# Kernel tuning notes

Hardware: AMD Instinct MI355X
Metric: run time of the kernel (lower is better)

Reference implementation:

```python
import jax, jax.numpy as jnp
import numpy as np

N, E, F, EF, D, G = 25000, 100000, 32, 8, 64, 1000


def setup_inputs() -> dict:
    key = jax.random.key(0)
    ks = jax.random.split(key, 32)
    p = lambda k, shape: (jax.random.normal(k, shape, jnp.float32) * 0.05)
    inp = {
        "x": jax.random.normal(ks[0], (N, F), jnp.float32),
        "edge_index": jax.random.randint(ks[1], (2, E), 0, N, jnp.int64 if jax.config.jax_enable_x64 else jnp.int32),
        "edge_attr": jax.random.uniform(ks[2], (E, EF), jnp.float32),
        "batch": jnp.sort(jax.random.randint(ks[3], (N,), 0, G, jnp.int32)),
        # lin0
        "W0": p(ks[4], (F, D)), "b0": p(ks[5], (D,)),
        # edge MLP: Linear(EF, D) -> ReLU -> Linear(D, D*D)
        "We1": p(ks[6], (EF, D)), "be1": p(ks[7], (D,)),
        "We2": p(ks[8], (D, D * D)), "be2": p(ks[9], (D * D,)),
        # NNConv root weight + bias
        "Wroot": p(ks[10], (D, D)), "bconv": p(ks[11], (D,)),
        # GRU (single layer): gate order r, z, n
        "Wi": p(ks[12], (3 * D, D)), "Wh": p(ks[13], (3 * D, D)),
        "bi": p(ks[14], (3 * D,)), "bh": p(ks[15], (3 * D,)),
        # heads
        "W11": p(ks[16], (D, D)), "b11": p(ks[17], (D,)),
        "W12": p(ks[18], (D, D)), "b12": p(ks[19], (D,)),
        "W13": p(ks[20], (D, 1)), "b13": p(ks[21], (1,)),
        "W21": p(ks[22], (D, D)), "b21": p(ks[23], (D,)),
        "W22": p(ks[24], (D, D)), "b22": p(ks[25], (D,)),
        "W23": p(ks[26], (D, 1)), "b23": p(ks[27], (1,)),
    }
    return inp


def reference(x, edge_index, edge_attr, batch,
              W0, b0, We1, be1, We2, be2, Wroot, bconv,
              Wi, Wh, bi, bh,
              W11, b11, W12, b12, W13, b13,
              W21, b21, W22, b22, W23, b23):
    src, dst = edge_index[0], edge_index[1]
    # lin0 + relu
    x1 = jax.nn.relu(x @ W0 + b0)                      # [N, D]
    h = x1                                              # GRU hidden init
    # NNConv: dynamic per-edge weight via edge MLP
    ew = (jax.nn.relu(edge_attr @ We1 + be1) @ We2 + be2).reshape(E, D, D)
    msg = jnp.einsum('ei,eio->eo', x1[src], ew)        # per-edge matmul
    agg = jax.ops.segment_sum(msg, dst, num_segments=N)
    x2 = jax.nn.relu(x1 @ Wroot + agg + bconv)         # [N, D]
    # GRU single step (torch gate order: r, z, n)
    gi = x2 @ Wi.T + bi
    gh = h @ Wh.T + bh
    r = jax.nn.sigmoid(gi[:, :D] + gh[:, :D])
    z = jax.nn.sigmoid(gi[:, D:2 * D] + gh[:, D:2 * D])
    n = jnp.tanh(gi[:, 2 * D:] + r * gh[:, 2 * D:])
    hn = (1.0 - z) * n + z * h                          # [N, D]
    # graph pooling (scatter_add over batch)
    pooled = jax.ops.segment_sum(hn, batch, num_segments=G)  # [G, D]
    # two MLP heads
    x_1 = jax.nn.relu(pooled @ W11 + b11)
    x_1 = jax.nn.relu(x_1 @ W12 + b12)
    x_1 = x_1 @ W13 + b13
    x_2 = jax.nn.relu(pooled @ W21 + b21)
    x_2 = jax.nn.relu(x_2 @ W22 + b22)
    x_2 = x_2 @ W23 + b23
    return jnp.concatenate([x_1, x_2], axis=1)          # [G, 2]
```

## Files before the change

### kernel.cpp

```cpp
#include <hip/hip_runtime.h>
#include <hip/hip_bf16.h>

#define NN 25000
#define NE 100000
#define FIN 32
#define DD 64
#define NG 1000

typedef unsigned short u16;
typedef __attribute__((ext_vector_type(8))) short short8;
typedef __attribute__((ext_vector_type(4))) float f32x4;

__device__ __forceinline__ float b2f(u16 u) {
    union { unsigned int i; float f; } v; v.i = ((unsigned int)u) << 16; return v.f;
}
__device__ __forceinline__ u16 f2b(float f) {
    __hip_bfloat16 h = __float2bfloat16(f);
    return __builtin_bit_cast(u16, h);
}
__device__ __forceinline__ bool idx_is_i64(const int* e) {
    return (e[1] == 0) & (e[3] == 0) & (e[5] == 0) & (e[7] == 0) & (e[9] == 0);
}
__device__ __forceinline__ int ld_src(const int* e, int i, bool i64) {
    return i64 ? e[2 * i] : e[i];
}
__device__ __forceinline__ int ld_dst(const int* e, int i, bool i64) {
    return i64 ? e[2 * (NE + i)] : e[NE + i];
}

__global__ __launch_bounds__(256) void k_pre(const float* __restrict__ x,
                                             const float* __restrict__ W0,
                                             const float* __restrict__ b0,
                                             u16* __restrict__ x1b,
                                             const float* __restrict__ We2,
                                             const float* __restrict__ be2,
                                             float* __restrict__ agg,
                                             float* __restrict__ pooled,
                                             u16* __restrict__ Bt2) {
    __shared__ float sW[FIN * DD];
    __shared__ float sx[4 * FIN];
    if (blockIdx.x < 6250) {
        int tid = threadIdx.x;
        for (int i = tid; i < FIN * DD; i += 256) sW[i] = W0[i];
        int nbase = blockIdx.x * 4;
        for (int i = tid; i < 4 * FIN; i += 256) {
            int nl = i >> 5, f = i & 31;
            int n = nbase + nl;
            sx[i] = (n < NN) ? x[n * FIN + f] : 0.f;
        }
        __syncthreads();
        int lane = tid & 63, nl = tid >> 6;
        int n = nbase + nl;
        if (n < NN) {
            float acc = b0[lane];
            #pragma unroll
            for (int f = 0; f < FIN; f++) acc += sx[nl * FIN + f] * sW[f * DD + lane];
            x1b[n * DD + lane] = f2b(fmaxf(acc, 0.f));
        }
    } else {
        int tid = (blockIdx.x - 6250) * 256 + threadIdx.x;
        int stride = 1024 * 256;
        for (int idx = tid; idx < 65 * 4096; idx += stride) {
            int kc = idx >> 12;
            int rem = idx & 4095;
            int f = rem >> 9;
            int ln = (rem >> 3) & 63;
            int j = idx & 7;
            int s = f >> 2, c = f & 3;
            int o = c * 16 + (ln & 15);
            int r = kc * 64 + s * 32 + (ln >> 4) * 8 + j;
            float v = (r < 4096) ? We2[(r >> 6) * 4096 + (r & 63) * 64 + o]
                                 : be2[(r - 4096) * 64 + o];
            Bt2[idx] = f2b(v);
        }
        for (int idx = tid; idx < NN * DD; idx += stride) agg[idx] = 0.f;
        for (int idx = tid; idx < NG * DD; idx += stride) pooled[idx] = 0.f;
    }
}

__global__ __launch_bounds__(512, 4) void k_msg(const float* __restrict__ ea,
                                                const int* __restrict__ eidx,
                                                const float* __restrict__ We1,
                                                const float* __restrict__ be1,
                                                const u16* __restrict__ x1b,
                                                const u16* __restrict__ Bt2,
                                                float* __restrict__ agg) {
    __shared__ __align__(16) u16 sX[128 * 72];
    __shared__ __align__(16) float sT[64 * 128];
    __shared__ float sWe1[8 * 64];
    __shared__ float sbe1[64];
    __shared__ int sDst[128];
    const int tid = threadIdx.x;
    const int lane = tid & 63, wv = tid >> 6;
    const int ll = lane & 15, quad = lane >> 4;
    const int rh = wv >> 2, cq = wv & 3;
    const int e0 = blockIdx.x * 128;
    const bool i64 = idx_is_i64(eidx);

    if (tid < 512) sWe1[tid] = We1[tid];
    if (tid < 64) sbe1[tid] = be1[tid];
    if (tid < 128) sDst[tid] = (e0 + tid < NE) ? ld_dst(eidx, e0 + tid, i64) : 0;

    const int el4 = tid >> 2, seg = tid & 3;
    const int eg4 = e0 + el4;
    {
        if (eg4 < NE) {
            int sv = ld_src(eidx, eg4, i64);
            const u16* xr = x1b + sv * 64 + seg * 16;
            *(uint4*)&sX[el4 * 72 + seg * 16]     = *(const uint4*)(xr);
            *(uint4*)&sX[el4 * 72 + seg * 16 + 8] = *(const uint4*)(xr + 8);
        } else {
            uint4 z = make_uint4(0, 0, 0, 0);
            *(uint4*)&sX[el4 * 72 + seg * 16]     = z;
            *(uint4*)&sX[el4 * 72 + seg * 16 + 8] = z;
        }
    }
    float eav[8];
    if (eg4 < NE) {
        f32x4 v0 = *(const f32x4*)(ea + eg4 * 8);
        f32x4 v1 = *(const f32x4*)(ea + eg4 * 8 + 4);
        #pragma unroll
        for (int f = 0; f < 4; f++) { eav[f] = v0[f]; eav[4 + f] = v1[f]; }
    } else {
        #pragma unroll
        for (int f = 0; f < 8; f++) eav[f] = 0.f;
    }
    __syncthreads();

    {
        int k0 = seg * 16;
        for (int kk = 0; kk < 16; kk++) {
            int k = k0 + kk;
            float acc = sbe1[k];
            #pragma unroll
            for (int f = 0; f < 8; f++) acc += eav[f] * sWe1[f * 64 + k];
            sT[k * 128 + el4] = (eg4 < NE) ? fmaxf(acc, 0.f) : 0.f;
        }
    }
    __syncthreads();

    short8 xa[4][2];
    #pragma unroll
    for (int rt = 0; rt < 4; rt++)
        #pragma unroll
        for (int s = 0; s < 2; s++)
            xa[rt][s] = *(const short8*)&sX[(rh * 64 + rt * 16 + ll) * 72 + s * 32 + quad * 8];

    f32x4 msg[4];
    #pragma unroll
    for (int rt = 0; rt < 4; rt++) msg[rt] = (f32x4){0.f, 0.f, 0.f, 0.f};

    const u16* gB0 = Bt2 + (0 * 4 + cq) * 512 + lane * 8;
    const u16* gB1 = Bt2 + (1 * 4 + cq) * 512 + lane * 8;

    short8 bf0 = *(const short8*)gB0;
    short8 bf1 = *(const short8*)gB1;
    const f32x4 zero = (f32x4){0.f, 0.f, 0.f, 0.f};

    for (int kc = 0; kc < 64; kc++) {
        short8 bn0 = *(const short8*)(gB0 + (kc + 1) * 4096);
        short8 bn1 = *(const short8*)(gB1 + (kc + 1) * 4096);

        f32x4 tk[4];
        #pragma unroll
        for (int rt = 0; rt < 4; rt++)
            tk[rt] = *(const f32x4*)&sT[kc * 128 + rh * 64 + rt * 16 + quad * 4];

        #pragma unroll
        for (int rt = 0; rt < 4; rt++) {
            f32x4 q = __builtin_amdgcn_mfma_f32_16x16x32_bf16(xa[rt][0], bf0, zero, 0, 0, 0);
            q = __builtin_amdgcn_mfma_f32_16x16x32_bf16(xa[rt][1], bf1, q, 0, 0, 0);
            #pragma unroll
            for (int r = 0; r < 4; r++) msg[rt][r] += tk[rt][r] * q[r];
        }
        bf0 = bn0; bf1 = bn1;
    }
    #pragma unroll
    for (int rt = 0; rt < 4; rt++) {
        f32x4 q = __builtin_amdgcn_mfma_f32_16x16x32_bf16(xa[rt][0], bf0, zero, 0, 0, 0);
        q = __builtin_amdgcn_mfma_f32_16x16x32_bf16(xa[rt][1], bf1, q, 0, 0, 0);
        #pragma unroll
        for (int r = 0; r < 4; r++) msg[rt][r] += q[r];
    }

    #pragma unroll
    for (int rt = 0; rt < 4; rt++) {
        #pragma unroll
        for (int r = 0; r < 4; r++) {
            int el = rh * 64 + rt * 16 + quad * 4 + r;
            int eg = e0 + el;
            if (eg < NE) {
                int d = sDst[el];
                atomicAdd(&agg[d * 64 + cq * 16 + ll], msg[rt][r]);
            }
        }
    }
}

__global__ __launch_bounds__(256) void k_gru(const u16* __restrict__ x1b,
                                             const float* __restrict__ agg,
                                             const float* __restrict__ Wroot,
                                             const float* __restrict__ bconv,
                                             const float* __restrict__ Wi,
                                             const float* __restrict__ Wh,
                                             const float* __restrict__ bi,
                                             const float* __restrict__ bh,
                                             const int* __restrict__ batch,
                                             float* __restrict__ pooled) {
    __shared__ __align__(16) u16 sWi[192 * 72];
    __shared__ __align__(16) u16 sWh[192 * 72];
    __shared__ __align__(16) u16 sX2[64 * 72];
    __shared__ int sBatch[64];
    const int tid = threadIdx.x;
    const int lane = tid & 63, wv = tid >> 6;
    const int ll = lane & 15, quad = lane >> 4;
    const int n0 = blockIdx.x * 64;

    for (int idx = tid; idx < 64 * 16; idx += 256) {
        int n = idx & 63, k4 = (idx >> 6) * 4;
        ushort4 a;
        a.x = f2b(Wroot[(k4 + 0) * 64 + n]);
        a.y = f2b(Wroot[(k4 + 1) * 64 + n]);
        a.z = f2b(Wroot[(k4 + 2) * 64 + n]);
        a.w = f2b(Wroot[(k4 + 3) * 64 + n]);
        *(ushort4*)&sWi[n * 72 + k4] = a;
    }
    if (tid < 64) {
        int n = n0 + tid;
        sBatch[tid] = (n < NN) ? batch[n] : -1;
    }
    __syncthreads();

    short8 ha[2];
    {
        int n = n0 + wv * 16 + ll;
        #pragma unroll
        for (int kc = 0; kc < 2; kc++) {
            if (n < NN) ha[kc] = *(const short8*)(x1b + n * 64 + kc * 32 + quad * 8);
            else        ha[kc] = (short8){0,0,0,0,0,0,0,0};
        }
    }
    f32x4 acc1[4];
    #pragma unroll
    for (int c = 0; c < 4; c++) acc1[c] = (f32x4){0.f, 0.f, 0.f, 0.f};
    #pragma unroll
    for (int kc = 0; kc < 2; kc++) {
        #pragma unroll
        for (int c = 0; c < 4; c++) {
            short8 b = *(const short8*)&sWi[(c * 16 + ll) * 72 + kc * 32 + quad * 8];
            acc1[c] = __builtin_amdgcn_mfma_f32_16x16x32_bf16(ha[kc], b, acc1[c], 0, 0, 0);
        }
    }
    #pragma unroll
    for (int c = 0; c < 4; c++) {
        int col = c * 16 + ll;
        float bcv = bconv[col];
        #pragma unroll
        for (int r = 0; r < 4; r++) {
            int row = wv * 16 + quad * 4 + r;
            int n = n0 + row;
            float v = 0.f;
            if (n < NN) v = fmaxf(acc1[c][r] + agg[n * 64 + col] + bcv, 0.f);
            sX2[row * 72 + col] = f2b(v);
        }
    }
    __syncthreads();

    for (int idx = tid; idx < 192 * 16; idx += 256) {
        int j = idx >> 4, i4 = (idx & 15) * 4;
        float4 wi4 = *(const float4*)&Wi[j * 64 + i4];
        float4 wh4 = *(const float4*)&Wh[j * 64 + i4];
        ushort4 a, b;
        a.x = f2b(wi4.x); a.y = f2b(wi4.y); a.z = f2b(wi4.z); a.w = f2b(wi4.w);
        b.x = f2b(wh4.x); b.y = f2b(wh4.y); b.z = f2b(wh4.z); b.w = f2b(wh4.w);
        *(ushort4*)&sWi[j * 72 + i4] = a;
        *(ushort4*)&sWh[j * 72 + i4] = b;
    }
    __syncthreads();

    short8 xa[2];
    #pragma unroll
    for (int kc = 0; kc < 2; kc++)
        xa[kc] = *(const short8*)&sX2[(wv * 16 + ll) * 72 + kc * 32 + quad * 8];

    f32x4 agi[12], agh[12];
    #pragma unroll
    for (int c = 0; c < 12; c++) { agi[c] = (f32x4){0.f,0.f,0.f,0.f}; agh[c] = (f32x4){0.f,0.f,0.f,0.f}; }
    #pragma unroll
    for (int kc = 0; kc < 2; kc++) {
        #pragma unroll
        for (int c = 0; c < 12; c++) {
            short8 bi8 = *(const short8*)&sWi[(c * 16 + ll) * 72 + kc * 32 + quad * 8];
            short8 bh8 = *(const short8*)&sWh[(c * 16 + ll) * 72 + kc * 32 + quad * 8];
            agi[c] = __builtin_amdgcn_mfma_f32_16x16x32_bf16(xa[kc], bi8, agi[c], 0, 0, 0);
            agh[c] = __builtin_amdgcn_mfma_f32_16x16x32_bf16(ha[kc], bh8, agh[c], 0, 0, 0);
        }
    }

    float hnv[4][4];
    #pragma unroll
    for (int c0 = 0; c0 < 4; c0++) {
        int d = c0 * 16 + ll;
        float bir = bi[d],        bhr = bh[d];
        float biz = bi[64 + d],   bhz = bh[64 + d];
        float bin = bi[128 + d],  bhn = bh[128 + d];
        #pragma unroll
        for (int r = 0; r < 4; r++) {
            int row = wv * 16 + quad * 4 + r;
            int n = n0 + row;
            float gir = agi[c0][r] + bir,     ghr = agh[c0][r] + bhr;
            float giz = agi[c0 + 4][r] + biz, ghz = agh[c0 + 4][r] + bhz;
            float gin = agi[c0 + 8][r] + bin, ghn = agh[c0 + 8][r] + bhn;
            float rg = 1.f / (1.f + __expf(-(gir + ghr)));
            float zg = 1.f / (1.f + __expf(-(giz + ghz)));
            float ng = tanhf(gin + rg * ghn);
            float hv = (n < NN) ? b2f(x1b[n * 64 + d]) : 0.f;
            hnv[c0][r] = (n < NN) ? ((1.f - zg) * ng + zg * hv) : 0.f;
        }
    }
    __syncthreads();

    float* hbuf = (float*)sWi;
    #pragma unroll
    for (int c0 = 0; c0 < 4; c0++) {
        int d = c0 * 16 + ll;
        #pragma unroll
        for (int r = 0; r < 4; r++) {
            int row = wv * 16 + quad * 4 + r;
            hbuf[row * 65 + d] = hnv[c0][r];
        }
    }
    __syncthreads();

    {
        int d = lane;
        float sum = 0.f;
        int pb = sBatch[wv * 16];
        #pragma unroll
        for (int rr = 0; rr < 16; rr++) {
            int row = wv * 16 + rr;
            int b = sBatch[row];
            float v = hbuf[row * 65 + d];
            if (b != pb) {
                if (pb >= 0) atomicAdd(&pooled[pb * 64 + d], sum);
                sum = v; pb = b;
            } else {
                sum += v;
            }
        }
        if (pb >= 0) atomicAdd(&pooled[pb * 64 + d], sum);
    }
}

__global__ __launch_bounds__(256) void k_heads(const float* __restrict__ pooled,
                                               const float* __restrict__ W11, const float* __restrict__ b11,
                                               const float* __restrict__ W12, const float* __restrict__ b12,
                                               const float* __restrict__ W13, const float* __restrict__ b13,
                                               const float* __restrict__ W21, const float* __restrict__ b21,
                                               const float* __restrict__ W22, const float* __restrict__ b22,
                                               const float* __restrict__ W23, const float* __restrict__ b23,
                                               float* __restrict__ out) {
    __shared__ float sV[4][64];
    __shared__ float sA[4][64];
    int tid = threadIdx.x, lane = tid & 63, wv = tid >> 6;
    int g = blockIdx.x * 4 + wv;
    if (g >= NG) return;
    float p = pooled[g * 64 + lane];
    sV[wv][lane] = p;
    float y[2];
    const float* W1s[2] = {W11, W21}; const float* b1s[2] = {b11, b21};
    const float* W2s[2] = {W12, W22}; const float* b2s[2] = {b12, b22};
    const float* W3s[2] = {W13, W23}; const float* b3s[2] = {b13, b23};
    #pragma unroll
    for (int hd = 0; hd < 2; hd++) {
        float a = b1s[hd][lane];
        #pragma unroll 8
        for (int i = 0; i < 64; i++) a += sV[wv][i] * W1s[hd][i * 64 + lane];
        a = fmaxf(a, 0.f);
        sA[wv][lane] = a;
        float a2 = b2s[hd][lane];
        #pragma unroll 8
        for (int i = 0; i < 64; i++) a2 += sA[wv][i] * W2s[hd][i * 64 + lane];
        a2 = fmaxf(a2, 0.f);
        float part = a2 * W3s[hd][lane];
        #pragma unroll
        for (int m = 32; m > 0; m >>= 1) part += __shfl_xor(part, m, 64);
        y[hd] = part + b3s[hd][0];
    }
    if (lane == 0) {
        out[g * 2 + 0] = y[0];
        out[g * 2 + 1] = y[1];
    }
}

extern "C" void kernel_launch(void* const* d_in, const int* in_sizes, int n_in,
                              void* d_out, int out_size, void* d_ws, size_t ws_size,
                              hipStream_t stream) {
    const float* x     = (const float*)d_in[0];
    const int* eidx    = (const int*)d_in[1];
    const float* ea    = (const float*)d_in[2];
    const int* batch   = (const int*)d_in[3];
    const float* W0    = (const float*)d_in[4];  const float* b0    = (const float*)d_in[5];
    const float* We1   = (const float*)d_in[6];  const float* be1   = (const float*)d_in[7];
    const float* We2   = (const float*)d_in[8];  const float* be2   = (const float*)d_in[9];
    const float* Wroot = (const float*)d_in[10]; const float* bconv = (const float*)d_in[11];
    const float* Wi    = (const float*)d_in[12]; const float* Wh    = (const float*)d_in[13];
    const float* bi    = (const float*)d_in[14]; const float* bh    = (const float*)d_in[15];
    const float* W11   = (const float*)d_in[16]; const float* b11   = (const float*)d_in[17];
    const float* W12   = (const float*)d_in[18]; const float* b12   = (const float*)d_in[19];
    const float* W13   = (const float*)d_in[20]; const float* b13   = (const float*)d_in[21];
    const float* W21   = (const float*)d_in[22]; const float* b21   = (const float*)d_in[23];
    const float* W22   = (const float*)d_in[24]; const float* b22   = (const float*)d_in[25];
    const float* W23   = (const float*)d_in[26]; const float* b23   = (const float*)d_in[27];
    float* out = (float*)d_out;

    char* ws = (char*)d_ws;
    float* agg    = (float*)(ws);
    u16*   x1b    = (u16*)(ws + 6400000);
    u16*   Bt2    = (u16*)(ws + 9600000);
    float* pooled = (float*)(ws + 10132480);

    hipLaunchKernelGGL(k_pre, dim3(7274), dim3(256), 0, stream,
                       x, W0, b0, x1b, We2, be2, agg, pooled, Bt2);
    hipLaunchKernelGGL(k_msg, dim3(782), dim3(512), 0, stream, ea, eidx, We1, be1, x1b, Bt2, agg);
    hipLaunchKernelGGL(k_gru, dim3(391), dim3(256), 0, stream, x1b, agg, Wroot, bconv,
                       Wi, Wh, bi, bh, batch, pooled);
    hipLaunchKernelGGL(k_heads, dim3(250), dim3(256), 0, stream, pooled,
                       W11, b11, W12, b12, W13, b13, W21, b21, W22, b22, W23, b23, out);
}
```

Baseline: 236.5 us.

## Halve k_msg block to 4 waves, each covering all 128 edges

The message kernel now runs 256 threads (4 waves) instead of 512. Each wave handles all 128 edges of the block for one 16-column output quarter, with 8 row tiles instead of 4. Each B fragment loaded from global memory is therefore reused across twice as many MFMAs, and the K loop is manually unrolled by two with ping-pong B registers. The cost is more live registers per thread (xa and msg double) and fewer waves per block to hide latency, which may reduce occupancy.

```diff
diff --git a/kernel.cpp b/kernel.cpp
--- a/kernel.cpp
+++ b/kernel.cpp
@@ -78,7 +78,7 @@
     }
 }
 
-__global__ __launch_bounds__(512, 4) void k_msg(const float* __restrict__ ea,
+__global__ __launch_bounds__(256, 3) void k_msg(const float* __restrict__ ea,
                                                 const int* __restrict__ eidx,
                                                 const float* __restrict__ We1,
                                                 const float* __restrict__ be1,
@@ -91,34 +91,35 @@
     __shared__ float sbe1[64];
     __shared__ int sDst[128];
     const int tid = threadIdx.x;
-    const int lane = tid & 63, wv = tid >> 6;
+    const int lane = tid & 63, cq = tid >> 6;
     const int ll = lane & 15, quad = lane >> 4;
-    const int rh = wv >> 2, cq = wv & 3;
     const int e0 = blockIdx.x * 128;
     const bool i64 = idx_is_i64(eidx);
 
-    if (tid < 512) sWe1[tid] = We1[tid];
+    for (int i = tid; i < 512; i += 256) sWe1[i] = We1[i];
     if (tid < 64) sbe1[tid] = be1[tid];
     if (tid < 128) sDst[tid] = (e0 + tid < NE) ? ld_dst(eidx, e0 + tid, i64) : 0;
 
-    const int el4 = tid >> 2, seg = tid & 3;
-    const int eg4 = e0 + el4;
+    const int el2 = tid >> 1, half = tid & 1;
+    const int eg2 = e0 + el2;
     {
-        if (eg4 < NE) {
-            int sv = ld_src(eidx, eg4, i64);
-            const u16* xr = x1b + sv * 64 + seg * 16;
-            *(uint4*)&sX[el4 * 72 + seg * 16]     = *(const uint4*)(xr);
-            *(uint4*)&sX[el4 * 72 + seg * 16 + 8] = *(const uint4*)(xr + 8);
+        uint4* dst = (uint4*)&sX[el2 * 72 + half * 32];
+        if (eg2 < NE) {
+            int sv = ld_src(eidx, eg2, i64);
+            const uint4* xr = (const uint4*)(x1b + sv * 64 + half * 32);
+            dst[0] = xr[0];
+            dst[1] = xr[1];
+            dst[2] = xr[2];
+            dst[3] = xr[3];
         } else {
             uint4 z = make_uint4(0, 0, 0, 0);
-            *(uint4*)&sX[el4 * 72 + seg * 16]     = z;
-            *(uint4*)&sX[el4 * 72 + seg * 16 + 8] = z;
+            dst[0] = z; dst[1] = z; dst[2] = z; dst[3] = z;
         }
     }
     float eav[8];
-    if (eg4 < NE) {
-        f32x4 v0 = *(const f32x4*)(ea + eg4 * 8);
-        f32x4 v1 = *(const f32x4*)(ea + eg4 * 8 + 4);
+    if (eg2 < NE) {
+        f32x4 v0 = *(const f32x4*)(ea + eg2 * 8);
+        f32x4 v1 = *(const f32x4*)(ea + eg2 * 8 + 4);
         #pragma unroll
         for (int f = 0; f < 4; f++) { eav[f] = v0[f]; eav[4 + f] = v1[f]; }
     } else {
@@ -128,66 +129,67 @@
     __syncthreads();
 
     {
-        int k0 = seg * 16;
-        for (int kk = 0; kk < 16; kk++) {
-            int k = k0 + kk;
+        int kbase = half * 32;
+        for (int kk = 0; kk < 32; kk++) {
+            int k = kbase + kk;
             float acc = sbe1[k];
             #pragma unroll
             for (int f = 0; f < 8; f++) acc += eav[f] * sWe1[f * 64 + k];
-            sT[k * 128 + el4] = (eg4 < NE) ? fmaxf(acc, 0.f) : 0.f;
-        }
-    }
-    __syncthreads();
-
-    short8 xa[4][2];
-    #pragma unroll
-    for (int rt = 0; rt < 4; rt++)
+            sT[k * 128 + el2] = (eg2 < NE) ? fmaxf(acc, 0.f) : 0.f;
+        }
+    }
+    __syncthreads();
+
+    short8 xa[8][2];
+    #pragma unroll
+    for (int rt = 0; rt < 8; rt++)
         #pragma unroll
         for (int s = 0; s < 2; s++)
-            xa[rt][s] = *(const short8*)&sX[(rh * 64 + rt * 16 + ll) * 72 + s * 32 + quad * 8];
-
-    f32x4 msg[4];
-    #pragma unroll
-    for (int rt = 0; rt < 4; rt++) msg[rt] = (f32x4){0.f, 0.f, 0.f, 0.f};
+            xa[rt][s] = *(const short8*)&sX[(rt * 16 + ll) * 72 + s * 32 + quad * 8];
+
+    f32x4 msg[8];
+    #pragma unroll
+    for (int rt = 0; rt < 8; rt++) msg[rt] = (f32x4){0.f, 0.f, 0.f, 0.f};
 
     const u16* gB0 = Bt2 + (0 * 4 + cq) * 512 + lane * 8;
     const u16* gB1 = Bt2 + (1 * 4 + cq) * 512 + lane * 8;
-
-    short8 bf0 = *(const short8*)gB0;
-    short8 bf1 = *(const short8*)gB1;
     const f32x4 zero = (f32x4){0.f, 0.f, 0.f, 0.f};
 
-    for (int kc = 0; kc < 64; kc++) {
-        short8 bn0 = *(const short8*)(gB0 + (kc + 1) * 4096);
-        short8 bn1 = *(const short8*)(gB1 + (kc + 1) * 4096);
-
-        f32x4 tk[4];
-        #pragma unroll
-        for (int rt = 0; rt < 4; rt++)
-            tk[rt] = *(const f32x4*)&sT[kc * 128 + rh * 64 + rt * 16 + quad * 4];
-
-        #pragma unroll
-        for (int rt = 0; rt < 4; rt++) {
-            f32x4 q = __builtin_amdgcn_mfma_f32_16x16x32_bf16(xa[rt][0], bf0, zero, 0, 0, 0);
-            q = __builtin_amdgcn_mfma_f32_16x16x32_bf16(xa[rt][1], bf1, q, 0, 0, 0);
-            #pragma unroll
-            for (int r = 0; r < 4; r++) msg[rt][r] += tk[rt][r] * q[r];
-        }
-        bf0 = bn0; bf1 = bn1;
-    }
-    #pragma unroll
-    for (int rt = 0; rt < 4; rt++) {
-        f32x4 q = __builtin_amdgcn_mfma_f32_16x16x32_bf16(xa[rt][0], bf0, zero, 0, 0, 0);
-        q = __builtin_amdgcn_mfma_f32_16x16x32_bf16(xa[rt][1], bf1, q, 0, 0, 0);
-        #pragma unroll
-        for (int r = 0; r < 4; r++) msg[rt][r] += q[r];
-    }
-
-    #pragma unroll
-    for (int rt = 0; rt < 4; rt++) {
+    short8 b0a = *(const short8*)gB0;
+    short8 b1a = *(const short8*)gB1;
+
+    for (int kc = 0; kc < 64; kc += 2) {
+        short8 b0b = *(const short8*)(gB0 + (kc + 1) * 4096);
+        short8 b1b = *(const short8*)(gB1 + (kc + 1) * 4096);
+        #pragma unroll
+        for (int rt = 0; rt < 8; rt++) {
+            f32x4 q = __builtin_amdgcn_mfma_f32_16x16x32_bf16(xa[rt][0], b0a, zero, 0, 0, 0);
+            q = __builtin_amdgcn_mfma_f32_16x16x32_bf16(xa[rt][1], b1a, q, 0, 0, 0);
+            f32x4 tk = *(const f32x4*)&sT[kc * 128 + rt * 16 + quad * 4];
+            msg[rt] += tk * q;
+        }
+        b0a = *(const short8*)(gB0 + (kc + 2) * 4096);
+        b1a = *(const short8*)(gB1 + (kc + 2) * 4096);
+        #pragma unroll
+        for (int rt = 0; rt < 8; rt++) {
+            f32x4 q = __builtin_amdgcn_mfma_f32_16x16x32_bf16(xa[rt][0], b0b, zero, 0, 0, 0);
+            q = __builtin_amdgcn_mfma_f32_16x16x32_bf16(xa[rt][1], b1b, q, 0, 0, 0);
+            f32x4 tk = *(const f32x4*)&sT[(kc + 1) * 128 + rt * 16 + quad * 4];
+            msg[rt] += tk * q;
+        }
+    }
+    #pragma unroll
+    for (int rt = 0; rt < 8; rt++) {
+        f32x4 q = __builtin_amdgcn_mfma_f32_16x16x32_bf16(xa[rt][0], b0a, zero, 0, 0, 0);
+        q = __builtin_amdgcn_mfma_f32_16x16x32_bf16(xa[rt][1], b1a, q, 0, 0, 0);
+        msg[rt] += q;
+    }
+
+    #pragma unroll
+    for (int rt = 0; rt < 8; rt++) {
         #pragma unroll
         for (int r = 0; r < 4; r++) {
-            int el = rh * 64 + rt * 16 + quad * 4 + r;
+            int el = rt * 16 + quad * 4 + r;
             int eg = e0 + el;
             if (eg < NE) {
                 int d = sDst[el];
@@ -422,7 +424,7 @@
 
     hipLaunchKernelGGL(k_pre, dim3(7274), dim3(256), 0, stream,
                        x, W0, b0, x1b, We2, be2, agg, pooled, Bt2);
-    hipLaunchKernelGGL(k_msg, dim3(782), dim3(512), 0, stream, ea, eidx, We1, be1, x1b, Bt2, agg);
+    hipLaunchKernelGGL(k_msg, dim3(782), dim3(256), 0, stream, ea, eidx, We1, be1, x1b, Bt2, agg);
     hipLaunchKernelGGL(k_gru, dim3(391), dim3(256), 0, stream, x1b, agg, Wroot, bconv,
                        Wi, Wh, bi, bh, batch, pooled);
     hipLaunchKernelGGL(k_heads, dim3(250), dim3(256), 0, stream, pooled,
```

After: 237.8 us. No clear change (+0.5%).

## Unroll message MFMA loop by two with independent accumulators and batch lin0 rows

Applied to the files above, without the earlier changes.

The per-edge message loop is unrolled by two k-chunks. Each step now issues two independent MFMAs instead of a chained pair, and the sT scale loads and next B fragments are prefetched a step ahead. The bias row is folded in as an extra sT row of ones, so the tail reuses the same code path. In k_pre each lin0 block now handles 16 nodes instead of 4, which cuts redundant W0 staging and block count, at the cost of more registers and a longer tail.

```diff
diff --git a/kernel.cpp b/kernel.cpp
--- a/kernel.cpp
+++ b/kernel.cpp
@@ -38,27 +38,32 @@
                                              float* __restrict__ pooled,
                                              u16* __restrict__ Bt2) {
     __shared__ float sW[FIN * DD];
-    __shared__ float sx[4 * FIN];
-    if (blockIdx.x < 6250) {
+    __shared__ float sx[16 * FIN];
+    if (blockIdx.x < 1563) {
         int tid = threadIdx.x;
         for (int i = tid; i < FIN * DD; i += 256) sW[i] = W0[i];
-        int nbase = blockIdx.x * 4;
-        for (int i = tid; i < 4 * FIN; i += 256) {
+        int nbase = blockIdx.x * 16;
+        for (int i = tid; i < 16 * FIN; i += 256) {
             int nl = i >> 5, f = i & 31;
             int n = nbase + nl;
             sx[i] = (n < NN) ? x[n * FIN + f] : 0.f;
         }
         __syncthreads();
         int lane = tid & 63, nl = tid >> 6;
-        int n = nbase + nl;
-        if (n < NN) {
-            float acc = b0[lane];
-            #pragma unroll
-            for (int f = 0; f < FIN; f++) acc += sx[nl * FIN + f] * sW[f * DD + lane];
-            x1b[n * DD + lane] = f2b(fmaxf(acc, 0.f));
+        float bias = b0[lane];
+        #pragma unroll
+        for (int rr = 0; rr < 4; rr++) {
+            int row = nl * 4 + rr;
+            int n = nbase + row;
+            if (n < NN) {
+                float acc = bias;
+                #pragma unroll
+                for (int f = 0; f < FIN; f++) acc += sx[row * FIN + f] * sW[f * DD + lane];
+                x1b[n * DD + lane] = f2b(fmaxf(acc, 0.f));
+            }
         }
     } else {
-        int tid = (blockIdx.x - 6250) * 256 + threadIdx.x;
+        int tid = (blockIdx.x - 1563) * 256 + threadIdx.x;
         int stride = 1024 * 256;
         for (int idx = tid; idx < 65 * 4096; idx += stride) {
             int kc = idx >> 12;
@@ -86,7 +91,7 @@
                                                 const u16* __restrict__ Bt2,
                                                 float* __restrict__ agg) {
     __shared__ __align__(16) u16 sX[128 * 72];
-    __shared__ __align__(16) float sT[64 * 128];
+    __shared__ __align__(16) float sT[65 * 128];
     __shared__ float sWe1[8 * 64];
     __shared__ float sbe1[64];
     __shared__ int sDst[128];
@@ -99,7 +104,10 @@
 
     if (tid < 512) sWe1[tid] = We1[tid];
     if (tid < 64) sbe1[tid] = be1[tid];
-    if (tid < 128) sDst[tid] = (e0 + tid < NE) ? ld_dst(eidx, e0 + tid, i64) : 0;
+    if (tid < 128) {
+        sDst[tid] = (e0 + tid < NE) ? ld_dst(eidx, e0 + tid, i64) : 0;
+        sT[64 * 128 + tid] = 1.0f;
+    }
 
     const int el4 = tid >> 2, seg = tid & 3;
     const int eg4 = e0 + el4;
@@ -152,35 +160,75 @@
 
     const u16* gB0 = Bt2 + (0 * 4 + cq) * 512 + lane * 8;
     const u16* gB1 = Bt2 + (1 * 4 + cq) * 512 + lane * 8;
-
-    short8 bf0 = *(const short8*)gB0;
-    short8 bf1 = *(const short8*)gB1;
     const f32x4 zero = (f32x4){0.f, 0.f, 0.f, 0.f};
-
-    for (int kc = 0; kc < 64; kc++) {
-        short8 bn0 = *(const short8*)(gB0 + (kc + 1) * 4096);
-        short8 bn1 = *(const short8*)(gB1 + (kc + 1) * 4096);
-
-        f32x4 tk[4];
+    const int tkoff = rh * 64 + quad * 4;
+
+    short8 c00 = *(const short8*)(gB0);
+    short8 c01 = *(const short8*)(gB1);
+    short8 c10 = *(const short8*)(gB0 + 4096);
+    short8 c11 = *(const short8*)(gB1 + 4096);
+    f32x4 tkA[4], tkB[4];
+    #pragma unroll
+    for (int rt = 0; rt < 4; rt++)
+        tkA[rt] = *(const f32x4*)&sT[tkoff + rt * 16];
+
+    for (int kc = 0; kc < 62; kc += 2) {
+        short8 n00 = *(const short8*)(gB0 + (kc + 2) * 4096);
+        short8 n01 = *(const short8*)(gB1 + (kc + 2) * 4096);
+        short8 n10 = *(const short8*)(gB0 + (kc + 3) * 4096);
+        short8 n11 = *(const short8*)(gB1 + (kc + 3) * 4096);
         #pragma unroll
         for (int rt = 0; rt < 4; rt++)
-            tk[rt] = *(const f32x4*)&sT[kc * 128 + rh * 64 + rt * 16 + quad * 4];
-
+            tkB[rt] = *(const f32x4*)&sT[(kc + 1) * 128 + tkoff + rt * 16];
         #pragma unroll
         for (int rt = 0; rt < 4; rt++) {
-            f32x4 q = __builtin_amdgcn_mfma_f32_16x16x32_bf16(xa[rt][0], bf0, zero, 0, 0, 0);
-            q = __builtin_amdgcn_mfma_f32_16x16x32_bf16(xa[rt][1], bf1, q, 0, 0, 0);
-            #pragma unroll
-            for (int r = 0; r < 4; r++) msg[rt][r] += tk[rt][r] * q[r];
-        }
-        bf0 = bn0; bf1 = bn1;
-    }
-    #pragma unroll
-    for (int rt = 0; rt < 4; rt++) {
-        f32x4 q = __builtin_amdgcn_mfma_f32_16x16x32_bf16(xa[rt][0], bf0, zero, 0, 0, 0);
-        q = __builtin_amdgcn_mfma_f32_16x16x32_bf16(xa[rt][1], bf1, q, 0, 0, 0);
-        #pragma unroll
-        for (int r = 0; r < 4; r++) msg[rt][r] += q[r];
+            f32x4 q0 = __builtin_amdgcn_mfma_f32_16x16x32_bf16(xa[rt][0], c00, zero, 0, 0, 0);
+            f32x4 q1 = __builtin_amdgcn_mfma_f32_16x16x32_bf16(xa[rt][1], c01, zero, 0, 0, 0);
+            msg[rt] += tkA[rt] * q0;
+            msg[rt] += tkA[rt] * q1;
+        }
+        #pragma unroll
+        for (int rt = 0; rt < 4; rt++)
+            tkA[rt] = *(const f32x4*)&sT[(kc + 2) * 128 + tkoff + rt * 16];
+        #pragma unroll
+        for (int rt = 0; rt < 4; rt++) {
+            f32x4 q0 = __builtin_amdgcn_mfma_f32_16x16x32_bf16(xa[rt][0], c10, zero, 0, 0, 0);
+            f32x4 q1 = __builtin_amdgcn_mfma_f32_16x16x32_bf16(xa[rt][1], c11, zero, 0, 0, 0);
+            msg[rt] += tkB[rt] * q0;
+            msg[rt] += tkB[rt] * q1;
+        }
+        c00 = n00; c01 = n01; c10 = n10; c11 = n11;
+    }
+    {
+        short8 n00 = *(const short8*)(gB0 + 64 * 4096);
+        short8 n01 = *(const short8*)(gB1 + 64 * 4096);
+        #pragma unroll
+        for (int rt = 0; rt < 4; rt++)
+            tkB[rt] = *(const f32x4*)&sT[63 * 128 + tkoff + rt * 16];
+        #pragma unroll
+        for (int rt = 0; rt < 4; rt++) {
+            f32x4 q0 = __builtin_amdgcn_mfma_f32_16x16x32_bf16(xa[rt][0], c00, zero, 0, 0, 0);
+            f32x4 q1 = __builtin_amdgcn_mfma_f32_16x16x32_bf16(xa[rt][1], c01, zero, 0, 0, 0);
+            msg[rt] += tkA[rt] * q0;
+            msg[rt] += tkA[rt] * q1;
+        }
+        #pragma unroll
+        for (int rt = 0; rt < 4; rt++)
+            tkA[rt] = *(const f32x4*)&sT[64 * 128 + tkoff + rt * 16];
+        #pragma unroll
+        for (int rt = 0; rt < 4; rt++) {
+            f32x4 q0 = __builtin_amdgcn_mfma_f32_16x16x32_bf16(xa[rt][0], c10, zero, 0, 0, 0);
+            f32x4 q1 = __builtin_amdgcn_mfma_f32_16x16x32_bf16(xa[rt][1], c11, zero, 0, 0, 0);
+            msg[rt] += tkB[rt] * q0;
+            msg[rt] += tkB[rt] * q1;
+        }
+        #pragma unroll
+        for (int rt = 0; rt < 4; rt++) {
+            f32x4 q0 = __builtin_amdgcn_mfma_f32_16x16x32_bf16(xa[rt][0], n00, zero, 0, 0, 0);
+            f32x4 q1 = __builtin_amdgcn_mfma_f32_16x16x32_bf16(xa[rt][1], n01, zero, 0, 0, 0);
+            msg[rt] += tkA[rt] * q0;
+            msg[rt] += tkA[rt] * q1;
+        }
     }
 
     #pragma unroll
@@ -420,7 +468,7 @@
     u16*   Bt2    = (u16*)(ws + 9600000);
     float* pooled = (float*)(ws + 10132480);
 
-    hipLaunchKernelGGL(k_pre, dim3(7274), dim3(256), 0, stream,
+    hipLaunchKernelGGL(k_pre, dim3(2587), dim3(256), 0, stream,
                        x, W0, b0, x1b, We2, be2, agg, pooled, Bt2);
     hipLaunchKernelGGL(k_msg, dim3(782), dim3(512), 0, stream, ea, eidx, We1, be1, x1b, Bt2, agg);
     hipLaunchKernelGGL(k_gru, dim3(391), dim3(256), 0, stream, x1b, agg, Wroot, bconv,
```

Measured after the change: 234.4 us. Within noise of the previous version (-0.9%).

## Load gathered x1 rows directly into registers and raise k_msg occupancy

Applied to the files above, without the earlier changes.

k_msg no longer stages gathered source rows in shared memory. Each lane loads its MFMA A-fragments straight from global x1b using source indices kept in shared memory, which removes the sX buffer and one LDS round trip. The bias row is folded into the main loop as a 65th k-step with t=1, the two MFMAs per step become independent, and the launch bound goes from 4 to 6 waves per SIMD, which may squeeze registers. k_pre also computes 16 nodes per block instead of 4, cutting its block count and the repeated W0 loads.

```diff
diff --git a/kernel.cpp b/kernel.cpp
--- a/kernel.cpp
+++ b/kernel.cpp
@@ -38,27 +38,32 @@
                                              float* __restrict__ pooled,
                                              u16* __restrict__ Bt2) {
     __shared__ float sW[FIN * DD];
-    __shared__ float sx[4 * FIN];
-    if (blockIdx.x < 6250) {
+    __shared__ float sx[16 * FIN];
+    if (blockIdx.x < 1563) {
         int tid = threadIdx.x;
         for (int i = tid; i < FIN * DD; i += 256) sW[i] = W0[i];
-        int nbase = blockIdx.x * 4;
-        for (int i = tid; i < 4 * FIN; i += 256) {
+        int nbase = blockIdx.x * 16;
+        for (int i = tid; i < 16 * FIN; i += 256) {
             int nl = i >> 5, f = i & 31;
             int n = nbase + nl;
             sx[i] = (n < NN) ? x[n * FIN + f] : 0.f;
         }
         __syncthreads();
         int lane = tid & 63, nl = tid >> 6;
-        int n = nbase + nl;
-        if (n < NN) {
-            float acc = b0[lane];
-            #pragma unroll
-            for (int f = 0; f < FIN; f++) acc += sx[nl * FIN + f] * sW[f * DD + lane];
-            x1b[n * DD + lane] = f2b(fmaxf(acc, 0.f));
+        float bias = b0[lane];
+        #pragma unroll
+        for (int rr = 0; rr < 4; rr++) {
+            int row = nl * 4 + rr;
+            int n = nbase + row;
+            if (n < NN) {
+                float acc = bias;
+                #pragma unroll
+                for (int f = 0; f < FIN; f++) acc += sx[row * FIN + f] * sW[f * DD + lane];
+                x1b[n * DD + lane] = f2b(fmaxf(acc, 0.f));
+            }
         }
     } else {
-        int tid = (blockIdx.x - 6250) * 256 + threadIdx.x;
+        int tid = (blockIdx.x - 1563) * 256 + threadIdx.x;
         int stride = 1024 * 256;
         for (int idx = tid; idx < 65 * 4096; idx += stride) {
             int kc = idx >> 12;
@@ -78,18 +83,18 @@
     }
 }
 
-__global__ __launch_bounds__(512, 4) void k_msg(const float* __restrict__ ea,
+__global__ __launch_bounds__(512, 6) void k_msg(const float* __restrict__ ea,
                                                 const int* __restrict__ eidx,
                                                 const float* __restrict__ We1,
                                                 const float* __restrict__ be1,
                                                 const u16* __restrict__ x1b,
                                                 const u16* __restrict__ Bt2,
                                                 float* __restrict__ agg) {
-    __shared__ __align__(16) u16 sX[128 * 72];
-    __shared__ __align__(16) float sT[64 * 128];
+    __shared__ __align__(16) float sT[65 * 128];
     __shared__ float sWe1[8 * 64];
     __shared__ float sbe1[64];
     __shared__ int sDst[128];
+    __shared__ int sSrc[128];
     const int tid = threadIdx.x;
     const int lane = tid & 63, wv = tid >> 6;
     const int ll = lane & 15, quad = lane >> 4;
@@ -97,24 +102,17 @@
     const int e0 = blockIdx.x * 128;
     const bool i64 = idx_is_i64(eidx);
 
-    if (tid < 512) sWe1[tid] = We1[tid];
+    sWe1[tid & 511] = We1[tid & 511];
     if (tid < 64) sbe1[tid] = be1[tid];
-    if (tid < 128) sDst[tid] = (e0 + tid < NE) ? ld_dst(eidx, e0 + tid, i64) : 0;
+    if (tid < 128) {
+        int e = e0 + tid;
+        sDst[tid] = (e < NE) ? ld_dst(eidx, e, i64) : 0;
+        sSrc[tid] = (e < NE) ? ld_src(eidx, e, i64) : 0;
+        sT[64 * 128 + tid] = 1.0f;
+    }
 
     const int el4 = tid >> 2, seg = tid & 3;
     const int eg4 = e0 + el4;
-    {
-        if (eg4 < NE) {
-            int sv = ld_src(eidx, eg4, i64);
-            const u16* xr = x1b + sv * 64 + seg * 16;
-            *(uint4*)&sX[el4 * 72 + seg * 16]     = *(const uint4*)(xr);
-            *(uint4*)&sX[el4 * 72 + seg * 16 + 8] = *(const uint4*)(xr + 8);
-        } else {
-            uint4 z = make_uint4(0, 0, 0, 0);
-            *(uint4*)&sX[el4 * 72 + seg * 16]     = z;
-            *(uint4*)&sX[el4 * 72 + seg * 16 + 8] = z;
-        }
-    }
     float eav[8];
     if (eg4 < NE) {
         f32x4 v0 = *(const f32x4*)(ea + eg4 * 8);
@@ -141,10 +139,12 @@
 
     short8 xa[4][2];
     #pragma unroll
-    for (int rt = 0; rt < 4; rt++)
-        #pragma unroll
-        for (int s = 0; s < 2; s++)
-            xa[rt][s] = *(const short8*)&sX[(rh * 64 + rt * 16 + ll) * 72 + s * 32 + quad * 8];
+    for (int rt = 0; rt < 4; rt++) {
+        int sv = sSrc[rh * 64 + rt * 16 + ll];
+        const u16* xr = x1b + sv * 64 + quad * 8;
+        xa[rt][0] = *(const short8*)(xr);
+        xa[rt][1] = *(const short8*)(xr + 32);
+    }
 
     f32x4 msg[4];
     #pragma unroll
@@ -152,35 +152,28 @@
 
     const u16* gB0 = Bt2 + (0 * 4 + cq) * 512 + lane * 8;
     const u16* gB1 = Bt2 + (1 * 4 + cq) * 512 + lane * 8;
-
-    short8 bf0 = *(const short8*)gB0;
-    short8 bf1 = *(const short8*)gB1;
     const f32x4 zero = (f32x4){0.f, 0.f, 0.f, 0.f};
-
-    for (int kc = 0; kc < 64; kc++) {
-        short8 bn0 = *(const short8*)(gB0 + (kc + 1) * 4096);
-        short8 bn1 = *(const short8*)(gB1 + (kc + 1) * 4096);
-
+    const int tkoff = rh * 64 + quad * 4;
+
+    short8 c0 = *(const short8*)(gB0);
+    short8 c1 = *(const short8*)(gB1);
+
+    for (int kc = 0; kc < 65; kc++) {
+        int kn = (kc < 64) ? kc + 1 : 64;
+        short8 n0 = *(const short8*)(gB0 + kn * 4096);
+        short8 n1 = *(const short8*)(gB1 + kn * 4096);
         f32x4 tk[4];
         #pragma unroll
         for (int rt = 0; rt < 4; rt++)
-            tk[rt] = *(const f32x4*)&sT[kc * 128 + rh * 64 + rt * 16 + quad * 4];
-
+            tk[rt] = *(const f32x4*)&sT[kc * 128 + tkoff + rt * 16];
         #pragma unroll
         for (int rt = 0; rt < 4; rt++) {
-            f32x4 q = __builtin_amdgcn_mfma_f32_16x16x32_bf16(xa[rt][0], bf0, zero, 0, 0, 0);
-            q = __builtin_amdgcn_mfma_f32_16x16x32_bf16(xa[rt][1], bf1, q, 0, 0, 0);
-            #pragma unroll
-            for (int r = 0; r < 4; r++) msg[rt][r] += tk[rt][r] * q[r];
-        }
-        bf0 = bn0; bf1 = bn1;
-    }
-    #pragma unroll
-    for (int rt = 0; rt < 4; rt++) {
-        f32x4 q = __builtin_amdgcn_mfma_f32_16x16x32_bf16(xa[rt][0], bf0, zero, 0, 0, 0);
-        q = __builtin_amdgcn_mfma_f32_16x16x32_bf16(xa[rt][1], bf1, q, 0, 0, 0);
-        #pragma unroll
-        for (int r = 0; r < 4; r++) msg[rt][r] += q[r];
+            f32x4 q0 = __builtin_amdgcn_mfma_f32_16x16x32_bf16(xa[rt][0], c0, zero, 0, 0, 0);
+            f32x4 q1 = __builtin_amdgcn_mfma_f32_16x16x32_bf16(xa[rt][1], c1, zero, 0, 0, 0);
+            msg[rt] += tk[rt] * q0;
+            msg[rt] += tk[rt] * q1;
+        }
+        c0 = n0; c1 = n1;
     }
 
     #pragma unroll
@@ -420,7 +413,7 @@
     u16*   Bt2    = (u16*)(ws + 9600000);
     float* pooled = (float*)(ws + 10132480);
 
-    hipLaunchKernelGGL(k_pre, dim3(7274), dim3(256), 0, stream,
+    hipLaunchKernelGGL(k_pre, dim3(2587), dim3(256), 0, stream,
                        x, W0, b0, x1b, We2, be2, agg, pooled, Bt2);
     hipLaunchKernelGGL(k_msg, dim3(782), dim3(512), 0, stream, ea, eidx, We1, be1, x1b, Bt2, agg);
     hipLaunchKernelGGL(k_gru, dim3(391), dim3(256), 0, stream, x1b, agg, Wroot, bconv,
```

Result: slower. 248.8 us (+5.2%).
